# Kernel optimization log

Measured on AMD Instinct MI355X. Metric: run time of the kernel, lower is better.

Reference implementation:

```python
import jax, jax.numpy as jnp
import numpy as np

M, N, DIM = 256, 256, 512
NITER = 1000
ALPHA = 0.3
SIGMA = max(M, N) / 2.0  # matches torch default sigma = max(m, n) / 2


def _locations():
    # Row-major 2-D grid coordinates, same order as SOM.neuron_locations()
    ii, jj = jnp.meshgrid(jnp.arange(M), jnp.arange(N), indexing='ij')
    return jnp.stack([ii.ravel(), jj.ravel()], axis=1)  # (M*N, 2) int32


def setup_inputs() -> dict:
    key = jax.random.key(0)
    k1, k2 = jax.random.split(key)
    return {
        'x': jax.random.normal(k1, (DIM,), dtype=jnp.float32),
        'weights': jax.random.normal(k2, (M * N, DIM), dtype=jnp.float32),
        'y': 3,     # label, only used for stats in the original; not in the math
        'it': 100,  # current iteration, controls alpha/sigma decay
    }


def reference(x, weights, y, it):
    locs = _locations()                                   # (M*N, 2)
    # BMU search: L2 distance from x to every neuron, argmin
    dists = jnp.linalg.norm(weights - x[None, :], axis=1)  # (M*N,)
    bmu_index = jnp.argmin(dists)
    bmu_loc = locs[bmu_index]                             # (2,)
    # Faithful to original: bmu_loc[0]*m + bmu_loc[1] (m == n here)
    bmu_1d = bmu_loc[0] * M + bmu_loc[1]
    winner = weights[bmu_1d]                              # (DIM,)
    # Linearly decaying learning rate / neighbourhood radius
    lr = 1.0 - it / NITER
    alpha_op = ALPHA * lr
    sigma_op = SIGMA * lr
    # Gaussian neighbourhood over squared grid distance to BMU
    d2 = jnp.sum((locs.astype(jnp.float32) - bmu_loc.astype(jnp.float32)) ** 2, axis=1)  # (M*N,)
    neigh = jnp.exp(-d2 / (sigma_op ** 2))
    # Weight update: w += alpha * h(i, bmu) * (x - w)
    new_weights = weights + (alpha_op * neigh)[:, None] * (x[None, :] - weights)
    return winner, new_weights
```

## Files before the change

### kernel.cpp

```cpp
#include <hip/hip_runtime.h>
#include <stdint.h>

#define MM   256
#define NN   256
#define DIMD 512
#define ROWS (MM * NN)

#define K1_BLOCKS 2048
#define WPB       4
#define ROWS_PER_WAVE 8

typedef float vfloat4 __attribute__((ext_vector_type(4)));

__global__ __launch_bounds__(256) void som_argmin_kernel(
    const float* __restrict__ x,
    const float* __restrict__ w,
    unsigned long long* __restrict__ slots)
{
    const int lane  = threadIdx.x & 63;
    const int wave  = threadIdx.x >> 6;
    const int gwave = blockIdx.x * WPB + wave;
    const int row0  = gwave * ROWS_PER_WAVE;

    const float4* x4 = reinterpret_cast<const float4*>(x);
    const float4 xa = x4[lane];
    const float4 xb = x4[lane + 64];

    float d[ROWS_PER_WAVE];

    #pragma unroll
    for (int r = 0; r < ROWS_PER_WAVE; ++r) {
        const float4* w4 =
            reinterpret_cast<const float4*>(w + (size_t)(row0 + r) * DIMD);
        const float4 wa = w4[lane];
        const float4 wb = w4[lane + 64];

        float s = 0.0f, t;
        t = wa.x - xa.x; s = fmaf(t, t, s);
        t = wa.y - xa.y; s = fmaf(t, t, s);
        t = wa.z - xa.z; s = fmaf(t, t, s);
        t = wa.w - xa.w; s = fmaf(t, t, s);
        t = wb.x - xb.x; s = fmaf(t, t, s);
        t = wb.y - xb.y; s = fmaf(t, t, s);
        t = wb.z - xb.z; s = fmaf(t, t, s);
        t = wb.w - xb.w; s = fmaf(t, t, s);
        d[r] = s;
    }

    #pragma unroll
    for (int off = 32; off > 0; off >>= 1) {
        #pragma unroll
        for (int r = 0; r < ROWS_PER_WAVE; ++r)
            d[r] += __shfl_xor(d[r], off, 64);
    }

    unsigned long long best = ~0ull;
    #pragma unroll
    for (int r = 0; r < ROWS_PER_WAVE; ++r) {
        unsigned long long key =
            (((unsigned long long)__float_as_uint(d[r])) << 32) |
            (unsigned long long)(unsigned)(row0 + r);
        best = (key < best) ? key : best;
    }

    __shared__ unsigned long long sbest[WPB];
    if (lane == 0) sbest[wave] = best;
    __syncthreads();
    if (threadIdx.x == 0) {
        unsigned long long b = sbest[0];
        #pragma unroll
        for (int i = 1; i < WPB; ++i) b = (sbest[i] < b) ? sbest[i] : b;
        slots[blockIdx.x] = b;
    }
}

__global__ __launch_bounds__(256) void som_update_kernel(
    const float* __restrict__ x,
    const float* __restrict__ w,
    const int* __restrict__ it_ptr,
    const unsigned long long* __restrict__ slots,
    float* __restrict__ out)
{
    const int lane  = threadIdx.x & 63;
    const int wave  = threadIdx.x >> 6;

    unsigned long long b = ~0ull;
    for (int i = threadIdx.x; i < K1_BLOCKS; i += 256) {
        unsigned long long v = slots[i];
        b = (v < b) ? v : b;
    }
    #pragma unroll
    for (int off = 32; off > 0; off >>= 1) {
        unsigned long long o = __shfl_xor(b, off, 64);
        b = (o < b) ? o : b;
    }
    __shared__ unsigned long long sbest[WPB];
    if (lane == 0) sbest[wave] = b;
    __syncthreads();
    unsigned long long g = sbest[0];
    #pragma unroll
    for (int i = 1; i < WPB; ++i) g = (sbest[i] < g) ? sbest[i] : g;

    const unsigned bmu = (unsigned)(g & 0xFFFFFFFFull);
    const float bi = (float)(bmu >> 8);
    const float bj = (float)(bmu & 255u);

    const double itd      = (double)(*it_ptr);
    const double lr       = 1.0 - itd / 1000.0;
    const float  alpha_op = (float)(0.3 * lr);
    const double sigma_op = 128.0 * lr;
    const float  inv_s2   = (float)(1.0 / (sigma_op * sigma_op));

    const float4* x4 = reinterpret_cast<const float4*>(x);
    const float4 xa = x4[lane];
    const float4 xb = x4[lane + 64];

    float* winner      = out;
    float* new_weights = out + DIMD;

    const int gwave = blockIdx.x * WPB + wave;
    const int row0  = gwave * ROWS_PER_WAVE;

    #pragma unroll
    for (int r = 0; r < ROWS_PER_WAVE; ++r) {
        const int row = row0 + r;
        const float di = (float)(row >> 8) - bi;
        const float dj = (float)(row & 255) - bj;
        const float d2 = di * di + dj * dj;
        const float coef = alpha_op * __expf(-d2 * inv_s2);

        const float4* w4 =
            reinterpret_cast<const float4*>(w + (size_t)row * DIMD);
        const float4 wa = w4[lane];
        const float4 wb = w4[lane + 64];

        vfloat4 oa, ob;
        oa.x = fmaf(coef, xa.x - wa.x, wa.x);
        oa.y = fmaf(coef, xa.y - wa.y, wa.y);
        oa.z = fmaf(coef, xa.z - wa.z, wa.z);
        oa.w = fmaf(coef, xa.w - wa.w, wa.w);
        ob.x = fmaf(coef, xb.x - wb.x, wb.x);
        ob.y = fmaf(coef, xb.y - wb.y, wb.y);
        ob.z = fmaf(coef, xb.z - wb.z, wb.z);
        ob.w = fmaf(coef, xb.w - wb.w, wb.w);

        vfloat4* o4 = reinterpret_cast<vfloat4*>(new_weights + (size_t)row * DIMD);
        __builtin_nontemporal_store(oa, o4 + lane);
        __builtin_nontemporal_store(ob, o4 + lane + 64);

        if (row == (int)bmu) {
            float4* wn = reinterpret_cast<float4*>(winner);
            wn[lane]      = wa;
            wn[lane + 64] = wb;
        }
    }
}

extern "C" void kernel_launch(void* const* d_in, const int* in_sizes, int n_in,
                              void* d_out, int out_size, void* d_ws, size_t ws_size,
                              hipStream_t stream) {
    const float* x       = (const float*)d_in[0];
    const float* weights = (const float*)d_in[1];
    const int*   it_ptr  = (const int*)d_in[3];

    float* out = (float*)d_out;
    unsigned long long* slots = (unsigned long long*)d_ws;

    som_argmin_kernel<<<K1_BLOCKS, 256, 0, stream>>>(x, weights, slots);
    som_update_kernel<<<K1_BLOCKS, 256, 0, stream>>>(x, weights, it_ptr, slots, out);
}
```

Measured before the change: 70.63 us.

## Fuse argmin and update into one cooperative kernel keeping weights on-chip

Replaces the two-kernel argmin-then-update pipeline with a single cooperative kernel of 512 blocks that reads each weight row once. Each wave holds its rows in registers, plus a few in LDS, across a grid-wide atomic barrier, then computes the BMU and writes the updated weights without rereading global memory. This halves the weight read traffic and removes one launch. In exchange it adds two memsets, a spin-wait grid barrier and heavy register/LDS pressure that may limit occupancy. The old two-kernel path is kept as a fallback if the cooperative launch fails.

```diff
diff --git a/kernel.cpp b/kernel.cpp
--- a/kernel.cpp
+++ b/kernel.cpp
@@ -1,16 +1,162 @@
 #include <hip/hip_runtime.h>
 #include <stdint.h>
 
-#define MM   256
-#define NN   256
 #define DIMD 512
-#define ROWS (MM * NN)
-
-#define K1_BLOCKS 2048
-#define WPB       4
-#define ROWS_PER_WAVE 8
+#define ROWS 65536
+
+#define GRID  512
+#define BLOCK 512
+#define WPB   8
+#define RPW   16
+#define REG_ROWS 12
+#define LDS_ROWS 4
+
+#define FB_BLOCKS 2048
+#define FB_WPB    4
+#define FB_RPW    8
 
 typedef float vfloat4 __attribute__((ext_vector_type(4)));
+
+__global__ __launch_bounds__(BLOCK, 4) void som_fused(
+    const float* __restrict__ x,
+    const float* __restrict__ w,
+    const int* __restrict__ it_ptr,
+    unsigned long long* __restrict__ slots,
+    int* __restrict__ bar,
+    float* __restrict__ out)
+{
+    __shared__ float lds[WPB * LDS_ROWS * DIMD];
+
+    const int lane = threadIdx.x & 63;
+    const int wave = threadIdx.x >> 6;
+    const int row0 = (blockIdx.x * WPB + wave) * RPW;
+
+    const float4* x4 = reinterpret_cast<const float4*>(x);
+    const float4 xa = x4[lane];
+    const float4 xb = x4[lane + 64];
+
+    float4 ra[REG_ROWS], rb[REG_ROWS];
+    unsigned long long best = ~0ull;
+
+    #pragma unroll
+    for (int r = 0; r < RPW; ++r) {
+        const float4* w4 =
+            reinterpret_cast<const float4*>(w + (size_t)(row0 + r) * DIMD);
+        const float4 wa = w4[lane];
+        const float4 wb = w4[lane + 64];
+        if (r < REG_ROWS) {
+            ra[r] = wa; rb[r] = wb;
+        } else {
+            float4* dst = reinterpret_cast<float4*>(
+                lds + (wave * LDS_ROWS + (r - REG_ROWS)) * DIMD);
+            dst[lane]      = wa;
+            dst[lane + 64] = wb;
+        }
+
+        float s = 0.0f, t;
+        t = wa.x - xa.x; s = fmaf(t, t, s);
+        t = wa.y - xa.y; s = fmaf(t, t, s);
+        t = wa.z - xa.z; s = fmaf(t, t, s);
+        t = wa.w - xa.w; s = fmaf(t, t, s);
+        t = wb.x - xb.x; s = fmaf(t, t, s);
+        t = wb.y - xb.y; s = fmaf(t, t, s);
+        t = wb.z - xb.z; s = fmaf(t, t, s);
+        t = wb.w - xb.w; s = fmaf(t, t, s);
+
+        #pragma unroll
+        for (int off = 32; off > 0; off >>= 1)
+            s += __shfl_xor(s, off, 64);
+
+        const unsigned long long key =
+            (((unsigned long long)__float_as_uint(s)) << 32) |
+            (unsigned long long)(unsigned)(row0 + r);
+        best = (key < best) ? key : best;
+    }
+
+    if (lane == 0) atomicMin(&slots[blockIdx.x], best);
+
+    __syncthreads();
+    if (threadIdx.x == 0) {
+        __threadfence();
+        const int old = __hip_atomic_fetch_add(&bar[0], 1, __ATOMIC_ACQ_REL,
+                                               __HIP_MEMORY_SCOPE_AGENT);
+        if (old == GRID - 1) {
+            __hip_atomic_store(&bar[1], 1, __ATOMIC_RELEASE,
+                               __HIP_MEMORY_SCOPE_AGENT);
+        } else {
+            while (__hip_atomic_load(&bar[1], __ATOMIC_ACQUIRE,
+                                     __HIP_MEMORY_SCOPE_AGENT) == 0) {
+                __builtin_amdgcn_s_sleep(2);
+            }
+        }
+        __threadfence();
+    }
+    __syncthreads();
+
+    unsigned long long g = ~0ull;
+    #pragma unroll
+    for (int k = 0; k < GRID / 64; ++k) {
+        const unsigned long long v = slots[k * 64 + lane];
+        g = (v < g) ? v : g;
+    }
+    #pragma unroll
+    for (int off = 32; off > 0; off >>= 1) {
+        const unsigned long long o = __shfl_xor(g, off, 64);
+        g = (o < g) ? o : g;
+    }
+
+    const unsigned bmu = (unsigned)(g & 0xFFFFFFFFull);
+    const float bi = (float)(bmu >> 8);
+    const float bj = (float)(bmu & 255u);
+
+    const double itd      = (double)(*it_ptr);
+    const double lr       = 1.0 - itd / 1000.0;
+    const float  alpha_op = (float)(0.3 * lr);
+    const double sigma_op = 128.0 * lr;
+    const float  inv_s2   = (float)(1.0 / (sigma_op * sigma_op));
+
+    float* winner      = out;
+    float* new_weights = out + DIMD;
+
+    #pragma unroll
+    for (int r = 0; r < RPW; ++r) {
+        const int row = row0 + r;
+        const float di = (float)(row >> 8) - bi;
+        const float dj = (float)(row & 255) - bj;
+        const float coef = alpha_op * __expf(-(di * di + dj * dj) * inv_s2);
+
+        float4 wa, wb;
+        if (r < REG_ROWS) {
+            wa = ra[r]; wb = rb[r];
+        } else {
+            const float4* src = reinterpret_cast<const float4*>(
+                lds + (wave * LDS_ROWS + (r - REG_ROWS)) * DIMD);
+            wa = src[lane];
+            wb = src[lane + 64];
+        }
+
+        vfloat4 oa, ob;
+        oa.x = fmaf(coef, xa.x - wa.x, wa.x);
+        oa.y = fmaf(coef, xa.y - wa.y, wa.y);
+        oa.z = fmaf(coef, xa.z - wa.z, wa.z);
+        oa.w = fmaf(coef, xa.w - wa.w, wa.w);
+        ob.x = fmaf(coef, xb.x - wb.x, wb.x);
+        ob.y = fmaf(coef, xb.y - wb.y, wb.y);
+        ob.z = fmaf(coef, xb.z - wb.z, wb.z);
+        ob.w = fmaf(coef, xb.w - wb.w, wb.w);
+
+        vfloat4* o4 =
+            reinterpret_cast<vfloat4*>(new_weights + (size_t)row * DIMD);
+        __builtin_nontemporal_store(oa, o4 + lane);
+        __builtin_nontemporal_store(ob, o4 + lane + 64);
+
+        if (row == (int)bmu) {
+            float4* wn = reinterpret_cast<float4*>(winner);
+            wn[lane]      = wa;
+            wn[lane + 64] = wb;
+        }
+    }
+}
 
 __global__ __launch_bounds__(256) void som_argmin_kernel(
     const float* __restrict__ x,
@@ -19,17 +165,17 @@
 {
     const int lane  = threadIdx.x & 63;
     const int wave  = threadIdx.x >> 6;
-    const int gwave = blockIdx.x * WPB + wave;
-    const int row0  = gwave * ROWS_PER_WAVE;
+    const int gwave = blockIdx.x * FB_WPB + wave;
+    const int row0  = gwave * FB_RPW;
 
     const float4* x4 = reinterpret_cast<const float4*>(x);
     const float4 xa = x4[lane];
     const float4 xb = x4[lane + 64];
 
-    float d[ROWS_PER_WAVE];
-
-    #pragma unroll
-    for (int r = 0; r < ROWS_PER_WAVE; ++r) {
+    float d[FB_RPW];
+
+    #pragma unroll
+    for (int r = 0; r < FB_RPW; ++r) {
         const float4* w4 =
             reinterpret_cast<const float4*>(w + (size_t)(row0 + r) * DIMD);
         const float4 wa = w4[lane];
@@ -50,26 +196,26 @@
     #pragma unroll
     for (int off = 32; off > 0; off >>= 1) {
         #pragma unroll
-        for (int r = 0; r < ROWS_PER_WAVE; ++r)
+        for (int r = 0; r < FB_RPW; ++r)
             d[r] += __shfl_xor(d[r], off, 64);
     }
 
     unsigned long long best = ~0ull;
     #pragma unroll
-    for (int r = 0; r < ROWS_PER_WAVE; ++r) {
+    for (int r = 0; r < FB_RPW; ++r) {
         unsigned long long key =
             (((unsigned long long)__float_as_uint(d[r])) << 32) |
             (unsigned long long)(unsigned)(row0 + r);
         best = (key < best) ? key : best;
     }
 
-    __shared__ unsigned long long sbest[WPB];
+    __shared__ unsigned long long sbest[FB_WPB];
     if (lane == 0) sbest[wave] = best;
     __syncthreads();
     if (threadIdx.x == 0) {
         unsigned long long b = sbest[0];
         #pragma unroll
-        for (int i = 1; i < WPB; ++i) b = (sbest[i] < b) ? sbest[i] : b;
+        for (int i = 1; i < FB_WPB; ++i) b = (sbest[i] < b) ? sbest[i] : b;
         slots[blockIdx.x] = b;
     }
 }
@@ -85,7 +231,7 @@
     const int wave  = threadIdx.x >> 6;
 
     unsigned long long b = ~0ull;
-    for (int i = threadIdx.x; i < K1_BLOCKS; i += 256) {
+    for (int i = threadIdx.x; i < FB_BLOCKS; i += 256) {
         unsigned long long v = slots[i];
         b = (v < b) ? v : b;
     }
@@ -94,12 +240,12 @@
         unsigned long long o = __shfl_xor(b, off, 64);
         b = (o < b) ? o : b;
     }
-    __shared__ unsigned long long sbest[WPB];
+    __shared__ unsigned long long sbest[FB_WPB];
     if (lane == 0) sbest[wave] = b;
     __syncthreads();
     unsigned long long g = sbest[0];
     #pragma unroll
-    for (int i = 1; i < WPB; ++i) g = (sbest[i] < g) ? sbest[i] : g;
+    for (int i = 1; i < FB_WPB; ++i) g = (sbest[i] < g) ? sbest[i] : g;
 
     const unsigned bmu = (unsigned)(g & 0xFFFFFFFFull);
     const float bi = (float)(bmu >> 8);
@@ -118,16 +264,15 @@
     float* winner      = out;
     float* new_weights = out + DIMD;
 
-    const int gwave = blockIdx.x * WPB + wave;
-    const int row0  = gwave * ROWS_PER_WAVE;
-
-    #pragma unroll
-    for (int r = 0; r < ROWS_PER_WAVE; ++r) {
+    const int gwave = blockIdx.x * FB_WPB + wave;
+    const int row0  = gwave * FB_RPW;
+
+    #pragma unroll
+    for (int r = 0; r < FB_RPW; ++r) {
         const int row = row0 + r;
         const float di = (float)(row >> 8) - bi;
         const float dj = (float)(row & 255) - bj;
-        const float d2 = di * di + dj * dj;
-        const float coef = alpha_op * __expf(-d2 * inv_s2);
+        const float coef = alpha_op * __expf(-(di * di + dj * dj) * inv_s2);
 
         const float4* w4 =
             reinterpret_cast<const float4*>(w + (size_t)row * DIMD);
@@ -162,10 +307,24 @@
     const float* x       = (const float*)d_in[0];
     const float* weights = (const float*)d_in[1];
     const int*   it_ptr  = (const int*)d_in[3];
-
     float* out = (float*)d_out;
-    unsigned long long* slots = (unsigned long long*)d_ws;
-
-    som_argmin_kernel<<<K1_BLOCKS, 256, 0, stream>>>(x, weights, slots);
-    som_update_kernel<<<K1_BLOCKS, 256, 0, stream>>>(x, weights, it_ptr, slots, out);
+
+    unsigned long long* slots  = (unsigned long long*)d_ws;
+    int*                bar    = (int*)((char*)d_ws + 4096);
+    unsigned long long* slots2 = (unsigned long long*)((char*)d_ws + 8192);
+
+    hipMemsetAsync(slots, 0xFF, GRID * sizeof(unsigned long long), stream);
+    hipMemsetAsync(bar, 0, 2 * sizeof(int), stream);
+
+    void* args[] = { (void*)&x, (void*)&weights, (void*)&it_ptr,
+                     (void*)&slots, (void*)&bar, (void*)&out };
+    hipError_t err = hipLaunchCooperativeKernel((const void*)som_fused,
+                                                dim3(GRID), dim3(BLOCK),
+                                                args, 0, stream);
+    if (err != hipSuccess) {
+        (void)hipGetLastError();
+        som_argmin_kernel<<<FB_BLOCKS, 256, 0, stream>>>(x, weights, slots2);
+        som_update_kernel<<<FB_BLOCKS, 256, 0, stream>>>(x, weights, it_ptr,
+                                                         slots2, out);
+    }
 }
```

Measured after the change: 195.9 us. +177.4%, slower.
